# Performance work log

Hardware: AMD Instinct MI355X
Metric: run time of the kernel (lower is better)

Reference implementation:

```python
import jax, jax.numpy as jnp
import numpy as np

B, N, D = 64, 8192, 128
IN, OUT, H = 64, 64, 512
NH_R, NH_W = 4, 4
GD_R = D + 6          # k, beta, g, s(3), gamma
GD_W = 3 * D + 6      # + erase, add
LSTM_IN = IN + OUT + NH_R * D
EPS = 1e-10


def setup_inputs() -> dict:
    key = jax.random.key(0)
    ks = jax.random.split(key, 18)
    f32 = jnp.float32

    def nrm(k, shape, scale=1.0):
        return (jax.random.normal(k, shape) * scale).astype(f32)

    mem_dev = 1.0 / float(np.sqrt(N + D))   # matches NTMMemory.initialize_memory scale
    return {
        'x_input': nrm(ks[0], (B, IN)),
        'prev_y': nrm(ks[1], (B, OUT)),
        'prev_read': nrm(ks[2], (B, NH_R * D), 0.1),
        'memory': nrm(ks[3], (B, N, D), mem_dev),
        'prev_w_read': jax.nn.softmax(nrm(ks[4], (B, NH_R, N)), axis=-1),
        'prev_w_write': jax.nn.softmax(nrm(ks[5], (B, NH_W, N)), axis=-1),
        'h0': nrm(ks[6], (B, H), 0.1),
        'c0': nrm(ks[7], (B, H), 0.1),
        'W_ih': nrm(ks[8], (4 * H, LSTM_IN), 1.0 / np.sqrt(LSTM_IN)),
        'W_hh': nrm(ks[9], (4 * H, H), 1.0 / np.sqrt(H)),
        'b_ih': jnp.zeros((4 * H,), f32),
        'b_hh': jnp.zeros((4 * H,), f32),
        'W_rhead': nrm(ks[10], (NH_R * GD_R, H), 1.0 / np.sqrt(H)),
        'b_rhead': jnp.zeros((NH_R * GD_R,), f32),
        'W_whead': nrm(ks[11], (NH_W * GD_W, H), 1.0 / np.sqrt(H)),
        'b_whead': jnp.zeros((NH_W * GD_W,), f32),
        'W_out': nrm(ks[12], (OUT, H + NH_R * D), 1.0 / np.sqrt(H + NH_R * D)),
        'b_out': jnp.zeros((OUT,), f32),
    }


def _address(ctrl, W, b, nh, gd, memory, prev_w):
    """Content + location addressing for nh heads. ctrl:[B,H] -> w:[B,nh,N]."""
    o = (ctrl @ W.T + b).reshape(ctrl.shape[0], nh, gd)
    k = o[..., :D]                                          # [B,nh,D]
    beta = jax.nn.softplus(o[..., D:D + 1])
    g = jax.nn.sigmoid(o[..., D + 1:D + 2])
    s = jax.nn.softmax(jax.nn.softplus(o[..., D + 2:D + 5]), axis=-1)  # 3-way shift
    gamma = 1.0 + jax.nn.softplus(o[..., D + 5:D + 6])
    # batched cosine similarity (replaces triple python loop in source)
    kn = k / (jnp.linalg.norm(k, axis=-1, keepdims=True) + EPS)
    mn = memory / (jnp.linalg.norm(memory, axis=-1, keepdims=True) + EPS)
    sim = jnp.einsum('bhd,bnd->bhn', kn, mn)                # [B,nh,N]
    wc = jax.nn.softmax(beta * sim, axis=-1)
    # interpolation + circular convolution shift (shifts -1,0,+1)
    wg = g * wc + (1.0 - g) * prev_w
    ws = (s[..., 0:1] * jnp.roll(wg, 1, axis=-1)
          + s[..., 1:2] * wg
          + s[..., 2:3] * jnp.roll(wg, -1, axis=-1))
    # sharpening
    wp = ws ** gamma
    w = wp / (jnp.sum(wp, axis=-1, keepdims=True) + EPS)
    return w, o


def reference(x_input, prev_y, prev_read, memory, prev_w_read, prev_w_write,
              h0, c0, W_ih, W_hh, b_ih, b_hh,
              W_rhead, b_rhead, W_whead, b_whead, W_out, b_out):
    # --- controller: one LSTM step (PyTorch gate order i,f,g,o) ---
    ctrl_in = jnp.concatenate([x_input, prev_y, prev_read], axis=-1)   # [B,LSTM_IN]
    gates = ctrl_in @ W_ih.T + b_ih + h0 @ W_hh.T + b_hh               # [B,4H]
    i, f, gg, o = jnp.split(gates, 4, axis=-1)
    c = jax.nn.sigmoid(f) * c0 + jax.nn.sigmoid(i) * jnp.tanh(gg)
    h = jax.nn.sigmoid(o) * jnp.tanh(c)
    # --- write heads: address then erase/add (batched outer products) ---
    w_w, ow = _address(h, W_whead, b_whead, NH_W, GD_W, memory, prev_w_write)
    erase = ow[..., D + 6:2 * D + 6]       # raw slices, as in source _generate_addressing
    add = ow[..., 2 * D + 6:3 * D + 6]
    mem = memory
    for hidx in range(NH_W):               # small fixed head count
        wv = w_w[:, hidx, :, None]         # [B,N,1]
        mem = mem * (1.0 - wv * erase[:, hidx, None, :]) + wv * add[:, hidx, None, :]
    # --- read heads ---
    w_r, _ = _address(h, W_rhead, b_rhead, NH_R, GD_R, mem, prev_w_read)
    r = jnp.einsum('bhn,bnd->bhd', w_r, mem)                # [B,NH_R,D]
    # --- external output fn ---
    ext_in = jnp.concatenate([h, r.reshape(r.shape[0], NH_R * D)], axis=-1)
    y = jnp.tanh(ext_in @ W_out.T + b_out)                  # [B,OUT]
    return (y, mem, h, c, w_r, w_w)
```

## Files before the change

### kernel.cpp

```cpp
#include <hip/hip_runtime.h>
#include <math.h>

#define B 64
#define N 8192
#define D 128
#define H 512
#define NHEAD 4
#define GDW 390
#define GDR 134
#define KL 1152
#define EPSF 1e-10f

__device__ __forceinline__ float softplusf(float x) {
    return x > 20.f ? x : log1pf(expf(x));
}
__device__ __forceinline__ float sigmoidf(float x) {
    return 1.f / (1.f + expf(-x));
}

__global__ void prep_xt(const float* __restrict__ x, const float* __restrict__ py,
                        const float* __restrict__ pr, const float* __restrict__ h0,
                        float* __restrict__ XT) {
    int idx = blockIdx.x * 256 + threadIdx.x;
    if (idx >= KL * B) return;
    int k = idx >> 6, b = idx & 63;
    float v;
    if (k < 64)       v = x[b * 64 + k];
    else if (k < 128) v = py[b * 64 + (k - 64)];
    else if (k < 640) v = pr[b * 512 + (k - 128)];
    else              v = h0[b * 512 + (k - 640)];
    XT[idx] = v;
}

__global__ __launch_bounds__(256) void controller(const float* __restrict__ XT,
        const float* __restrict__ W_ih, const float* __restrict__ W_hh,
        const float* __restrict__ b_ih, const float* __restrict__ b_hh,
        float* __restrict__ gatesT) {
    __shared__ float xs[64 * 64];
    int tid = threadIdx.x;
    int lane = tid & 63;
    int wave = tid >> 6;
    int j0 = blockIdx.x * 16 + wave * 4;
    float acc[4] = {0.f, 0.f, 0.f, 0.f};
    for (int k0 = 0; k0 < KL; k0 += 64) {
        __syncthreads();
        #pragma unroll
        for (int i = 0; i < 16; i++) xs[tid + i * 256] = XT[k0 * 64 + tid + i * 256];
        __syncthreads();
        const float* wp[4];
        #pragma unroll
        for (int jj = 0; jj < 4; jj++) {
            int j = j0 + jj;
            wp[jj] = (k0 < 640) ? (W_ih + j * 640 + k0) : (W_hh + j * 512 + (k0 - 640));
        }
        #pragma unroll 4
        for (int k = 0; k < 64; k++) {
            float xv = xs[k * 64 + lane];
            #pragma unroll
            for (int jj = 0; jj < 4; jj++) acc[jj] = fmaf(wp[jj][k], xv, acc[jj]);
        }
    }
    #pragma unroll
    for (int jj = 0; jj < 4; jj++) {
        int j = j0 + jj;
        gatesT[j * 64 + lane] = acc[jj] + b_ih[j] + b_hh[j];
    }
}

__global__ void lstm_cell(const float* __restrict__ gatesT, const float* __restrict__ c0,
                          float* __restrict__ h_out, float* __restrict__ c_out,
                          float* __restrict__ HT) {
    int tid = blockIdx.x * 256 + threadIdx.x;
    int b = tid >> 9, u = tid & 511;
    float gi = gatesT[u * 64 + b];
    float gf = gatesT[(512 + u) * 64 + b];
    float gg = gatesT[(1024 + u) * 64 + b];
    float go = gatesT[(1536 + u) * 64 + b];
    float c = sigmoidf(gf) * c0[b * 512 + u] + sigmoidf(gi) * tanhf(gg);
    float h = sigmoidf(go) * tanhf(c);
    c_out[b * 512 + u] = c;
    h_out[b * 512 + u] = h;
    HT[u * 64 + b] = h;
}

__global__ __launch_bounds__(256) void head_proj(const float* __restrict__ HT,
        const float* __restrict__ W_w, const float* __restrict__ W_r,
        const float* __restrict__ b_w, const float* __restrict__ b_r,
        float* __restrict__ o_w, float* __restrict__ o_r) {
    __shared__ float xs[64 * 64];
    int tid = threadIdx.x;
    int lane = tid & 63;
    int wave = tid >> 6;
    int j0 = blockIdx.x * 16 + wave * 4;
    float acc[4] = {0.f, 0.f, 0.f, 0.f};
    const float* wp[4];
    #pragma unroll
    for (int jj = 0; jj < 4; jj++) {
        int j = j0 + jj;
        wp[jj] = (j < 1560) ? (W_w + j * 512) : (W_r + (j - 1560) * 512);
    }
    for (int k0 = 0; k0 < 512; k0 += 64) {
        __syncthreads();
        #pragma unroll
        for (int i = 0; i < 16; i++) xs[tid + i * 256] = HT[k0 * 64 + tid + i * 256];
        __syncthreads();
        #pragma unroll 4
        for (int k = 0; k < 64; k++) {
            float xv = xs[k * 64 + lane];
            #pragma unroll
            for (int jj = 0; jj < 4; jj++) acc[jj] = fmaf(wp[jj][k0 + k], xv, acc[jj]);
        }
    }
    #pragma unroll
    for (int jj = 0; jj < 4; jj++) {
        int j = j0 + jj;
        if (j < 1560) o_w[lane * 1560 + j] = acc[jj] + b_w[j];
        else          o_r[lane * 536 + (j - 1560)] = acc[jj] + b_r[j - 1560];
    }
}

__global__ __launch_bounds__(128) void head_params(const float* __restrict__ o_w,
        const float* __restrict__ o_r, float* __restrict__ knw, float* __restrict__ knr,
        float* __restrict__ pw, float* __restrict__ prd, float* __restrict__ rzero) {
    __shared__ float red[2];
    int id = blockIdx.x;
    if (id < 256) rzero[id * 128 + threadIdx.x] = 0.f;
    bool isw = id < 256;
    int bh = isw ? id : id - 256;
    const float* o = isw ? (o_w + (bh >> 2) * 1560 + (bh & 3) * GDW)
                         : (o_r + (bh >> 2) * 536 + (bh & 3) * GDR);
    float* kn = (isw ? knw : knr) + bh * 128;
    float* pp = (isw ? pw : prd) + bh * 6;
    int t = threadIdx.x;
    float kv = o[t];
    float ss = kv * kv;
    #pragma unroll
    for (int m = 1; m < 64; m <<= 1) ss += __shfl_xor(ss, m);
    if ((t & 63) == 0) red[t >> 6] = ss;
    __syncthreads();
    float norm = sqrtf(red[0] + red[1]);
    kn[t] = kv / (norm + EPSF);
    if (t == 0) {
        float beta = softplusf(o[128]);
        float g = sigmoidf(o[129]);
        float s0 = softplusf(o[130]), s1 = softplusf(o[131]), s2 = softplusf(o[132]);
        float mx = fmaxf(s0, fmaxf(s1, s2));
        float e0 = expf(s0 - mx), e1 = expf(s1 - mx), e2 = expf(s2 - mx);
        float inv = 1.f / (e0 + e1 + e2);
        float gamma = 1.f + softplusf(o[133]);
        pp[0] = beta; pp[1] = g; pp[2] = e0 * inv; pp[3] = e1 * inv; pp[4] = e2 * inv; pp[5] = gamma;
    }
}

__global__ __launch_bounds__(256) void sim_write(const float* __restrict__ mem,
        const float* __restrict__ knw, float* __restrict__ sim) {
    int t = threadIdx.x;
    int lane = t & 63;
    int wv = t >> 6;
    int j = lane & 15;
    int u = lane >> 4;
    int b = blockIdx.x >> 7;
    int nb = (blockIdx.x & 127) * 64 + wv * 16 + u;
    float4 k[4][2];
    #pragma unroll
    for (int h = 0; h < 4; h++) {
        #pragma unroll
        for (int s = 0; s < 2; s++)
            k[h][s] = *(const float4*)(knw + (b * 4 + h) * 128 + s * 64 + j * 4);
    }
    #pragma unroll
    for (int it = 0; it < 4; it++) {
        int n = nb + it * 4;
        size_t base = ((size_t)b * N + n) * D + j * 4;
        const float4 m0 = *(const float4*)(mem + base);
        const float4 m1 = *(const float4*)(mem + base + 64);
        float s0 = m0.x*k[0][0].x + m0.y*k[0][0].y + m0.z*k[0][0].z + m0.w*k[0][0].w
                 + m1.x*k[0][1].x + m1.y*k[0][1].y + m1.z*k[0][1].z + m1.w*k[0][1].w;
        float s1 = m0.x*k[1][0].x + m0.y*k[1][0].y + m0.z*k[1][0].z + m0.w*k[1][0].w
                 + m1.x*k[1][1].x + m1.y*k[1][1].y + m1.z*k[1][1].z + m1.w*k[1][1].w;
        float s2 = m0.x*k[2][0].x + m0.y*k[2][0].y + m0.z*k[2][0].z + m0.w*k[2][0].w
                 + m1.x*k[2][1].x + m1.y*k[2][1].y + m1.z*k[2][1].z + m1.w*k[2][1].w;
        float s3 = m0.x*k[3][0].x + m0.y*k[3][0].y + m0.z*k[3][0].z + m0.w*k[3][0].w
                 + m1.x*k[3][1].x + m1.y*k[3][1].y + m1.z*k[3][1].z + m1.w*k[3][1].w;
        float nn = m0.x*m0.x + m0.y*m0.y + m0.z*m0.z + m0.w*m0.w
                 + m1.x*m1.x + m1.y*m1.y + m1.z*m1.z + m1.w*m1.w;
        s0 += __shfl_xor(s0, 1); s1 += __shfl_xor(s1, 1);
        s2 += __shfl_xor(s2, 1); s3 += __shfl_xor(s3, 1); nn += __shfl_xor(nn, 1);
        float p01 = (j & 1) ? s1 : s0;
        float p23 = (j & 1) ? s3 : s2;
        p01 += __shfl_xor(p01, 2); p23 += __shfl_xor(p23, 2); nn += __shfl_xor(nn, 2);
        float q = (j & 2) ? p23 : p01;
        q += __shfl_xor(q, 4);  nn += __shfl_xor(nn, 4);
        q += __shfl_xor(q, 8);  nn += __shfl_xor(nn, 8);
        if (j < 4) sim[((size_t)(b * 4 + j)) * N + n] = q / (sqrtf(nn) + EPSF);
    }
}

__global__ __launch_bounds__(512) void addr_finalize(const float* __restrict__ sim,
        const float* __restrict__ prev_w, const float* __restrict__ par,
        float* __restrict__ w_out) {
    __shared__ float buf[N];
    __shared__ float pbuf[N];
    __shared__ float red[8];
    int bh = blockIdx.x;
    int t = threadIdx.x;
    const float* s = sim + (size_t)bh * N;
    const float* pw = prev_w + (size_t)bh * N;
    float beta = par[bh * 6 + 0], g = par[bh * 6 + 1];
    float s0 = par[bh * 6 + 2], s1 = par[bh * 6 + 3], s2 = par[bh * 6 + 4];
    float gamma = par[bh * 6 + 5];
    float mx = -INFINITY;
    for (int i = t; i < N; i += 512) {
        float e = beta * s[i];
        buf[i] = e;
        mx = fmaxf(mx, e);
    }
    #pragma unroll
    for (int m = 1; m < 64; m <<= 1) mx = fmaxf(mx, __shfl_xor(mx, m));
    if ((t & 63) == 0) red[t >> 6] = mx;
    __syncthreads();
    mx = red[0];
    #pragma unroll
    for (int kk = 1; kk < 8; kk++) mx = fmaxf(mx, red[kk]);
    float sum = 0.f;
    for (int i = t; i < N; i += 512) {
        float v = expf(buf[i] - mx);
        buf[i] = v;
        sum += v;
    }
    #pragma unroll
    for (int m = 1; m < 64; m <<= 1) sum += __shfl_xor(sum, m);
    __syncthreads();
    if ((t & 63) == 0) red[t >> 6] = sum;
    __syncthreads();
    sum = red[0] + red[1] + red[2] + red[3] + red[4] + red[5] + red[6] + red[7];
    float inv = 1.f / sum;
    for (int i = t; i < N; i += 512) buf[i] = g * (buf[i] * inv) + (1.f - g) * pw[i];
    __syncthreads();
    float psum = 0.f;
    for (int i = t; i < N; i += 512) {
        float wsv = s0 * buf[(i + N - 1) & (N - 1)] + s1 * buf[i] + s2 * buf[(i + 1) & (N - 1)];
        float pv = powf(wsv, gamma);
        pbuf[i] = pv;
        psum += pv;
    }
    #pragma unroll
    for (int m = 1; m < 64; m <<= 1) psum += __shfl_xor(psum, m);
    __syncthreads();
    if ((t & 63) == 0) red[t >> 6] = psum;
    __syncthreads();
    psum = red[0] + red[1] + red[2] + red[3] + red[4] + red[5] + red[6] + red[7];
    float rinv = 1.f / (psum + EPSF);
    for (int i = t; i < N; i += 512) w_out[(size_t)bh * N + i] = pbuf[i] * rinv;
}

__global__ __launch_bounds__(256) void mem_update(const float* __restrict__ mem_in,
        const float* __restrict__ o_w, const float* __restrict__ w_w,
        const float* __restrict__ knr, float* __restrict__ mem_out,
        float* __restrict__ simr) {
    __shared__ float wlds[4][64];
    int t = threadIdx.x;
    int l = t & 31;
    int rg = t >> 5;
    int b = blockIdx.x >> 7;
    int n0 = (blockIdx.x & 127) * 64;
    {
        int h = t >> 6, idx = t & 63;
        wlds[h][idx] = w_w[((size_t)(b * 4 + h)) * N + n0 + idx];
    }
    float4 e[4], a[4], kr[4];
    #pragma unroll
    for (int h = 0; h < 4; h++) {
        const float* ob = o_w + b * 1560 + h * GDW;
        e[h].x = ob[134 + l * 4 + 0]; e[h].y = ob[134 + l * 4 + 1];
        e[h].z = ob[134 + l * 4 + 2]; e[h].w = ob[134 + l * 4 + 3];
        a[h].x = ob[262 + l * 4 + 0]; a[h].y = ob[262 + l * 4 + 1];
        a[h].z = ob[262 + l * 4 + 2]; a[h].w = ob[262 + l * 4 + 3];
        kr[h] = *(const float4*)(knr + (b * 4 + h) * 128 + l * 4);
    }
    __syncthreads();
    for (int it = 0; it < 8; it++) {
        int n = n0 + it * 8 + rg;
        size_t base = ((size_t)b * N + n) * D + l * 4;
        float4 m = *(const float4*)(mem_in + base);
        #pragma unroll
        for (int h = 0; h < 4; h++) {
            float wv = wlds[h][it * 8 + rg];
            m.x = m.x * (1.f - wv * e[h].x) + wv * a[h].x;
            m.y = m.y * (1.f - wv * e[h].y) + wv * a[h].y;
            m.z = m.z * (1.f - wv * e[h].z) + wv * a[h].z;
            m.w = m.w * (1.f - wv * e[h].w) + wv * a[h].w;
        }
        *(float4*)(mem_out + base) = m;
        float s0 = m.x * kr[0].x + m.y * kr[0].y + m.z * kr[0].z + m.w * kr[0].w;
        float s1 = m.x * kr[1].x + m.y * kr[1].y + m.z * kr[1].z + m.w * kr[1].w;
        float s2 = m.x * kr[2].x + m.y * kr[2].y + m.z * kr[2].z + m.w * kr[2].w;
        float s3 = m.x * kr[3].x + m.y * kr[3].y + m.z * kr[3].z + m.w * kr[3].w;
        float nn = m.x * m.x + m.y * m.y + m.z * m.z + m.w * m.w;
        s0 += __shfl_xor(s0, 1); s1 += __shfl_xor(s1, 1);
        s2 += __shfl_xor(s2, 1); s3 += __shfl_xor(s3, 1); nn += __shfl_xor(nn, 1);
        float p01 = (l & 1) ? s1 : s0;
        float p23 = (l & 1) ? s3 : s2;
        p01 += __shfl_xor(p01, 2); p23 += __shfl_xor(p23, 2); nn += __shfl_xor(nn, 2);
        float q = (l & 2) ? p23 : p01;
        q += __shfl_xor(q, 4); nn += __shfl_xor(nn, 4);
        float z = (l & 4) ? nn : q;
        z += __shfl_xor(z, 8);
        z += __shfl_xor(z, 16);
        float nnv = __shfl_xor(z, 4);
        if (l < 4) simr[((size_t)(b * 4 + l)) * N + n] = z / (sqrtf(nnv) + EPSF);
    }
}

__global__ __launch_bounds__(256) void read_vec(const float* __restrict__ mem,
        const float* __restrict__ w_r, float* __restrict__ r) {
    __shared__ float lds[8 * 512];
    __shared__ float wlds[4][512];
    int t = threadIdx.x;
    int l = t & 31;
    int rg = t >> 5;
    int b = blockIdx.x >> 4;
    int n0 = (blockIdx.x & 15) * 512;
    for (int i = t; i < 2048; i += 256) {
        int h = i >> 9, idx = i & 511;
        wlds[h][idx] = w_r[((size_t)(b * 4 + h)) * N + n0 + idx];
    }
    __syncthreads();
    float4 acc[4];
    #pragma unroll
    for (int h = 0; h < 4; h++) acc[h] = make_float4(0.f, 0.f, 0.f, 0.f);
    for (int it = 0; it < 64; it++) {
        int nl = it * 8 + rg;
        const float4 m = *(const float4*)(mem + ((size_t)b * N + n0 + nl) * D + l * 4);
        #pragma unroll
        for (int h = 0; h < 4; h++) {
            float wv = wlds[h][nl];
            acc[h].x += wv * m.x;
            acc[h].y += wv * m.y;
            acc[h].z += wv * m.z;
            acc[h].w += wv * m.w;
        }
    }
    #pragma unroll
    for (int h = 0; h < 4; h++) *(float4*)(lds + rg * 512 + h * 128 + l * 4) = acc[h];
    __syncthreads();
    for (int o = t; o < 512; o += 256) {
        float sum = 0.f;
        #pragma unroll
        for (int g2 = 0; g2 < 8; g2++) sum += lds[g2 * 512 + o];
        atomicAdd(&r[b * 512 + o], sum);
    }
}

__global__ __launch_bounds__(64) void out_y(const float* __restrict__ h,
        const float* __restrict__ r, const float* __restrict__ W_out,
        const float* __restrict__ b_out, float* __restrict__ y) {
    int b = blockIdx.x >> 6;
    int j = blockIdx.x & 63;
    int l = threadIdx.x;
    float acc = 0.f;
    #pragma unroll
    for (int kk = 0; kk < 16; kk++) {
        int k = l + kk * 64;
        float x = (k < 512) ? h[b * 512 + k] : r[b * 512 + (k - 512)];
        acc = fmaf(W_out[j * 1024 + k], x, acc);
    }
    #pragma unroll
    for (int m = 1; m < 64; m <<= 1) acc += __shfl_xor(acc, m);
    if (l == 0) y[b * 64 + j] = tanhf(acc + b_out[j]);
}

extern "C" void kernel_launch(void* const* d_in, const int* in_sizes, int n_in,
                              void* d_out, int out_size, void* d_ws, size_t ws_size,
                              hipStream_t stream) {
    const float* x_input      = (const float*)d_in[0];
    const float* prev_y       = (const float*)d_in[1];
    const float* prev_read    = (const float*)d_in[2];
    const float* memory       = (const float*)d_in[3];
    const float* prev_w_read  = (const float*)d_in[4];
    const float* prev_w_write = (const float*)d_in[5];
    const float* h0           = (const float*)d_in[6];
    const float* c0           = (const float*)d_in[7];
    const float* W_ih         = (const float*)d_in[8];
    const float* W_hh         = (const float*)d_in[9];
    const float* b_ih         = (const float*)d_in[10];
    const float* b_hh         = (const float*)d_in[11];
    const float* W_rhead      = (const float*)d_in[12];
    const float* b_rhead      = (const float*)d_in[13];
    const float* W_whead      = (const float*)d_in[14];
    const float* b_whead      = (const float*)d_in[15];
    const float* W_out        = (const float*)d_in[16];
    const float* b_out        = (const float*)d_in[17];

    float* out = (float*)d_out;
    float* y_o   = out;
    float* mem_o = out + 4096;
    float* h_o   = out + 4096 + 67108864;
    float* c_o   = h_o + 32768;
    float* wr_o  = c_o + 32768;
    float* ww_o  = wr_o + 2097152;

    float* ws     = (float*)d_ws;
    float* XT     = ws;
    float* HT     = XT + 73728;
    float* gatesT = HT + 32768;
    float* o_w    = gatesT + 131072;
    float* o_r    = o_w + 99840;
    float* knw    = o_r + 34304;
    float* knr    = knw + 32768;
    float* pw     = knr + 32768;
    float* prd    = pw + 1536;
    float* sim_w  = prd + 1536;
    float* sim_r  = sim_w + 2097152;
    float* r_ws   = sim_r + 2097152;

    prep_xt<<<288, 256, 0, stream>>>(x_input, prev_y, prev_read, h0, XT);
    controller<<<128, 256, 0, stream>>>(XT, W_ih, W_hh, b_ih, b_hh, gatesT);
    lstm_cell<<<128, 256, 0, stream>>>(gatesT, c0, h_o, c_o, HT);
    head_proj<<<131, 256, 0, stream>>>(HT, W_whead, W_rhead, b_whead, b_rhead, o_w, o_r);
    head_params<<<512, 128, 0, stream>>>(o_w, o_r, knw, knr, pw, prd, r_ws);
    sim_write<<<8192, 256, 0, stream>>>(memory, knw, sim_w);
    addr_finalize<<<256, 512, 0, stream>>>(sim_w, prev_w_write, pw, ww_o);
    mem_update<<<8192, 256, 0, stream>>>(memory, o_w, ww_o, knr, mem_o, sim_r);
    addr_finalize<<<256, 512, 0, stream>>>(sim_r, prev_w_read, prd, wr_o);
    read_vec<<<1024, 256, 0, stream>>>(mem_o, wr_o, r_ws);
    out_y<<<4096, 64, 0, stream>>>(h_o, r_ws, W_out, b_out, y_o);
}
```

Measured before the change: 756.5 us.

## Fuse memory addressing, update and read stages into one cooperative persistent kernel

Replaces the five-kernel sequence (write similarity, write addressing, memory update, read addressing, read vector) with one cooperative kernel of 1024 blocks, separated by grid syncs. Each block owns a fixed 512-row slice of one batch's memory, so a block reads back the same slice in later phases, which may hit in cache, and four launches are removed. The addressing routine also drops to 256 threads and recomputes powf in its last pass instead of keeping a second 32 KB LDS buffer, which cuts shared-memory use. The costs are grid-wide barriers, only 256 of 1024 blocks doing work in the addressing phases, and a reliance on cooperative launch, with an occupancy check and a fallback to the old kernels.

```diff
diff --git a/kernel.cpp b/kernel.cpp
--- a/kernel.cpp
+++ b/kernel.cpp
@@ -1,5 +1,8 @@
 #include <hip/hip_runtime.h>
+#include <hip/hip_cooperative_groups.h>
 #include <math.h>
+
+namespace cg = cooperative_groups;
 
 #define B 64
 #define N 8192
@@ -149,6 +152,208 @@
         float inv = 1.f / (e0 + e1 + e2);
         float gamma = 1.f + softplusf(o[133]);
         pp[0] = beta; pp[1] = g; pp[2] = e0 * inv; pp[3] = e1 * inv; pp[4] = e2 * inv; pp[5] = gamma;
+    }
+}
+
+__device__ void addr_phase(float* __restrict__ buf, float* __restrict__ red,
+                           const float* __restrict__ sim, const float* __restrict__ prevw,
+                           const float* __restrict__ par, float* __restrict__ w_out,
+                           int bh, int t) {
+    const float* s = sim + (size_t)bh * N;
+    const float* pwp = prevw + (size_t)bh * N;
+    float beta = par[bh * 6 + 0], g = par[bh * 6 + 1];
+    float s0 = par[bh * 6 + 2], s1 = par[bh * 6 + 3], s2 = par[bh * 6 + 4];
+    float gamma = par[bh * 6 + 5];
+    float mx = -INFINITY;
+    for (int i = t; i < N; i += 256) {
+        float e = beta * s[i];
+        buf[i] = e;
+        mx = fmaxf(mx, e);
+    }
+    #pragma unroll
+    for (int m = 1; m < 64; m <<= 1) mx = fmaxf(mx, __shfl_xor(mx, m));
+    if ((t & 63) == 0) red[t >> 6] = mx;
+    __syncthreads();
+    mx = fmaxf(fmaxf(red[0], red[1]), fmaxf(red[2], red[3]));
+    float sum = 0.f;
+    for (int i = t; i < N; i += 256) {
+        float v = expf(buf[i] - mx);
+        buf[i] = v;
+        sum += v;
+    }
+    #pragma unroll
+    for (int m = 1; m < 64; m <<= 1) sum += __shfl_xor(sum, m);
+    __syncthreads();
+    if ((t & 63) == 0) red[t >> 6] = sum;
+    __syncthreads();
+    sum = red[0] + red[1] + red[2] + red[3];
+    float inv = 1.f / sum;
+    for (int i = t; i < N; i += 256) buf[i] = g * (buf[i] * inv) + (1.f - g) * pwp[i];
+    __syncthreads();
+    float psum = 0.f;
+    for (int i = t; i < N; i += 256) {
+        float wsv = s0 * buf[(i + N - 1) & (N - 1)] + s1 * buf[i] + s2 * buf[(i + 1) & (N - 1)];
+        psum += powf(wsv, gamma);
+    }
+    #pragma unroll
+    for (int m = 1; m < 64; m <<= 1) psum += __shfl_xor(psum, m);
+    __syncthreads();
+    if ((t & 63) == 0) red[t >> 6] = psum;
+    __syncthreads();
+    psum = red[0] + red[1] + red[2] + red[3];
+    float rinv = 1.f / (psum + EPSF);
+    for (int i = t; i < N; i += 256) {
+        float wsv = s0 * buf[(i + N - 1) & (N - 1)] + s1 * buf[i] + s2 * buf[(i + 1) & (N - 1)];
+        w_out[(size_t)bh * N + i] = powf(wsv, gamma) * rinv;
+    }
+}
+
+__global__ __launch_bounds__(256, 4) void ntm_coop(
+        const float* __restrict__ mem_in, const float* __restrict__ knw,
+        const float* __restrict__ knr, const float* __restrict__ o_w,
+        const float* __restrict__ pw, const float* __restrict__ prd,
+        const float* __restrict__ pww, const float* __restrict__ pwr,
+        float* __restrict__ sim_w, float* __restrict__ sim_r,
+        float* __restrict__ ww_o, float* __restrict__ wr_o,
+        float* __restrict__ mem_o, float* __restrict__ r_ws) {
+    cg::grid_group grid = cg::this_grid();
+    __shared__ float smem[8448];
+    int t = threadIdx.x;
+    int blk = blockIdx.x;
+    int b = blk >> 4, part = blk & 15;
+    int n0 = part * 512;
+
+    {
+        int lane = t & 63, wv2 = t >> 6, j = lane & 15, u = lane >> 4;
+        float4 k[4][2];
+        #pragma unroll
+        for (int h = 0; h < 4; h++) {
+            #pragma unroll
+            for (int sgm = 0; sgm < 2; sgm++)
+                k[h][sgm] = *(const float4*)(knw + (b * 4 + h) * 128 + sgm * 64 + j * 4);
+        }
+        int rbase = n0 + wv2 * 16 + u;
+        for (int q = 0; q < 32; q++) {
+            int n = rbase + (q >> 2) * 64 + (q & 3) * 4;
+            size_t base = ((size_t)b * N + n) * D + j * 4;
+            const float4 m0 = *(const float4*)(mem_in + base);
+            const float4 m1 = *(const float4*)(mem_in + base + 64);
+            float s0 = m0.x*k[0][0].x + m0.y*k[0][0].y + m0.z*k[0][0].z + m0.w*k[0][0].w
+                     + m1.x*k[0][1].x + m1.y*k[0][1].y + m1.z*k[0][1].z + m1.w*k[0][1].w;
+            float s1 = m0.x*k[1][0].x + m0.y*k[1][0].y + m0.z*k[1][0].z + m0.w*k[1][0].w
+                     + m1.x*k[1][1].x + m1.y*k[1][1].y + m1.z*k[1][1].z + m1.w*k[1][1].w;
+            float s2 = m0.x*k[2][0].x + m0.y*k[2][0].y + m0.z*k[2][0].z + m0.w*k[2][0].w
+                     + m1.x*k[2][1].x + m1.y*k[2][1].y + m1.z*k[2][1].z + m1.w*k[2][1].w;
+            float s3 = m0.x*k[3][0].x + m0.y*k[3][0].y + m0.z*k[3][0].z + m0.w*k[3][0].w
+                     + m1.x*k[3][1].x + m1.y*k[3][1].y + m1.z*k[3][1].z + m1.w*k[3][1].w;
+            float nn = m0.x*m0.x + m0.y*m0.y + m0.z*m0.z + m0.w*m0.w
+                     + m1.x*m1.x + m1.y*m1.y + m1.z*m1.z + m1.w*m1.w;
+            s0 += __shfl_xor(s0, 1); s1 += __shfl_xor(s1, 1);
+            s2 += __shfl_xor(s2, 1); s3 += __shfl_xor(s3, 1); nn += __shfl_xor(nn, 1);
+            float p01 = (j & 1) ? s1 : s0;
+            float p23 = (j & 1) ? s3 : s2;
+            p01 += __shfl_xor(p01, 2); p23 += __shfl_xor(p23, 2); nn += __shfl_xor(nn, 2);
+            float qv = (j & 2) ? p23 : p01;
+            qv += __shfl_xor(qv, 4);  nn += __shfl_xor(nn, 4);
+            qv += __shfl_xor(qv, 8);  nn += __shfl_xor(nn, 8);
+            if (j < 4) sim_w[((size_t)(b * 4 + j)) * N + n] = qv / (sqrtf(nn) + EPSF);
+        }
+    }
+    __threadfence();
+    grid.sync();
+
+    if (blk < 256) addr_phase(smem, smem + 8192, sim_w, pww, pw, ww_o, blk, t);
+    __threadfence();
+    grid.sync();
+
+    {
+        for (int i = t; i < 2048; i += 256) {
+            int h = i >> 9, idx = i & 511;
+            smem[i] = ww_o[((size_t)(b * 4 + h)) * N + n0 + idx];
+        }
+        int l = t & 31, rg = t >> 5;
+        float4 e[4], a[4], kr[4];
+        #pragma unroll
+        for (int h = 0; h < 4; h++) {
+            const float* ob = o_w + b * 1560 + h * GDW;
+            e[h].x = ob[134 + l * 4 + 0]; e[h].y = ob[134 + l * 4 + 1];
+            e[h].z = ob[134 + l * 4 + 2]; e[h].w = ob[134 + l * 4 + 3];
+            a[h].x = ob[262 + l * 4 + 0]; a[h].y = ob[262 + l * 4 + 1];
+            a[h].z = ob[262 + l * 4 + 2]; a[h].w = ob[262 + l * 4 + 3];
+            kr[h] = *(const float4*)(knr + (b * 4 + h) * 128 + l * 4);
+        }
+        __syncthreads();
+        for (int it = 0; it < 64; it++) {
+            int nl = it * 8 + rg;
+            int n = n0 + nl;
+            size_t base = ((size_t)b * N + n) * D + l * 4;
+            float4 m = *(const float4*)(mem_in + base);
+            #pragma unroll
+            for (int h = 0; h < 4; h++) {
+                float wv = smem[h * 512 + nl];
+                m.x = m.x * (1.f - wv * e[h].x) + wv * a[h].x;
+                m.y = m.y * (1.f - wv * e[h].y) + wv * a[h].y;
+                m.z = m.z * (1.f - wv * e[h].z) + wv * a[h].z;
+                m.w = m.w * (1.f - wv * e[h].w) + wv * a[h].w;
+            }
+            *(float4*)(mem_o + base) = m;
+            float s0 = m.x * kr[0].x + m.y * kr[0].y + m.z * kr[0].z + m.w * kr[0].w;
+            float s1 = m.x * kr[1].x + m.y * kr[1].y + m.z * kr[1].z + m.w * kr[1].w;
+            float s2 = m.x * kr[2].x + m.y * kr[2].y + m.z * kr[2].z + m.w * kr[2].w;
+            float s3 = m.x * kr[3].x + m.y * kr[3].y + m.z * kr[3].z + m.w * kr[3].w;
+            float nn = m.x * m.x + m.y * m.y + m.z * m.z + m.w * m.w;
+            s0 += __shfl_xor(s0, 1); s1 += __shfl_xor(s1, 1);
+            s2 += __shfl_xor(s2, 1); s3 += __shfl_xor(s3, 1); nn += __shfl_xor(nn, 1);
+            float p01 = (l & 1) ? s1 : s0;
+            float p23 = (l & 1) ? s3 : s2;
+            p01 += __shfl_xor(p01, 2); p23 += __shfl_xor(p23, 2); nn += __shfl_xor(nn, 2);
+            float qv = (l & 2) ? p23 : p01;
+            qv += __shfl_xor(qv, 4); nn += __shfl_xor(nn, 4);
+            float z = (l & 4) ? nn : qv;
+            z += __shfl_xor(z, 8);
+            z += __shfl_xor(z, 16);
+            float nnv = __shfl_xor(z, 4);
+            if (l < 4) sim_r[((size_t)(b * 4 + l)) * N + n] = z / (sqrtf(nnv) + EPSF);
+        }
+    }
+    __threadfence();
+    grid.sync();
+
+    if (blk < 256) addr_phase(smem, smem + 8192, sim_r, pwr, prd, wr_o, blk, t);
+    __threadfence();
+    grid.sync();
+
+    {
+        for (int i = t; i < 2048; i += 256) {
+            int h = i >> 9, idx = i & 511;
+            smem[4096 + i] = wr_o[((size_t)(b * 4 + h)) * N + n0 + idx];
+        }
+        __syncthreads();
+        int l = t & 31, rg = t >> 5;
+        float4 acc[4];
+        #pragma unroll
+        for (int h = 0; h < 4; h++) acc[h] = make_float4(0.f, 0.f, 0.f, 0.f);
+        for (int it = 0; it < 64; it++) {
+            int nl = it * 8 + rg;
+            const float4 m = *(const float4*)(mem_o + ((size_t)b * N + n0 + nl) * D + l * 4);
+            #pragma unroll
+            for (int h = 0; h < 4; h++) {
+                float wv = smem[4096 + h * 512 + nl];
+                acc[h].x += wv * m.x;
+                acc[h].y += wv * m.y;
+                acc[h].z += wv * m.z;
+                acc[h].w += wv * m.w;
+            }
+        }
+        #pragma unroll
+        for (int h = 0; h < 4; h++) *(float4*)(smem + rg * 512 + h * 128 + l * 4) = acc[h];
+        __syncthreads();
+        for (int o = t; o < 512; o += 256) {
+            float sum = 0.f;
+            #pragma unroll
+            for (int g2 = 0; g2 < 8; g2++) sum += smem[g2 * 512 + o];
+            atomicAdd(&r_ws[b * 512 + o], sum);
+        }
     }
 }
 
@@ -196,62 +401,12 @@
     }
 }
 
-__global__ __launch_bounds__(512) void addr_finalize(const float* __restrict__ sim,
+__global__ __launch_bounds__(256) void addr_finalize(const float* __restrict__ sim,
         const float* __restrict__ prev_w, const float* __restrict__ par,
         float* __restrict__ w_out) {
     __shared__ float buf[N];
-    __shared__ float pbuf[N];
-    __shared__ float red[8];
-    int bh = blockIdx.x;
-    int t = threadIdx.x;
-    const float* s = sim + (size_t)bh * N;
-    const float* pw = prev_w + (size_t)bh * N;
-    float beta = par[bh * 6 + 0], g = par[bh * 6 + 1];
-    float s0 = par[bh * 6 + 2], s1 = par[bh * 6 + 3], s2 = par[bh * 6 + 4];
-    float gamma = par[bh * 6 + 5];
-    float mx = -INFINITY;
-    for (int i = t; i < N; i += 512) {
-        float e = beta * s[i];
-        buf[i] = e;
-        mx = fmaxf(mx, e);
-    }
-    #pragma unroll
-    for (int m = 1; m < 64; m <<= 1) mx = fmaxf(mx, __shfl_xor(mx, m));
-    if ((t & 63) == 0) red[t >> 6] = mx;
-    __syncthreads();
-    mx = red[0];
-    #pragma unroll
-    for (int kk = 1; kk < 8; kk++) mx = fmaxf(mx, red[kk]);
-    float sum = 0.f;
-    for (int i = t; i < N; i += 512) {
-        float v = expf(buf[i] - mx);
-        buf[i] = v;
-        sum += v;
-    }
-    #pragma unroll
-    for (int m = 1; m < 64; m <<= 1) sum += __shfl_xor(sum, m);
-    __syncthreads();
-    if ((t & 63) == 0) red[t >> 6] = sum;
-    __syncthreads();
-    sum = red[0] + red[1] + red[2] + red[3] + red[4] + red[5] + red[6] + red[7];
-    float inv = 1.f / sum;
-    for (int i = t; i < N; i += 512) buf[i] = g * (buf[i] * inv) + (1.f - g) * pw[i];
-    __syncthreads();
-    float psum = 0.f;
-    for (int i = t; i < N; i += 512) {
-        float wsv = s0 * buf[(i + N - 1) & (N - 1)] + s1 * buf[i] + s2 * buf[(i + 1) & (N - 1)];
-        float pv = powf(wsv, gamma);
-        pbuf[i] = pv;
-        psum += pv;
-    }
-    #pragma unroll
-    for (int m = 1; m < 64; m <<= 1) psum += __shfl_xor(psum, m);
-    __syncthreads();
-    if ((t & 63) == 0) red[t >> 6] = psum;
-    __syncthreads();
-    psum = red[0] + red[1] + red[2] + red[3] + red[4] + red[5] + red[6] + red[7];
-    float rinv = 1.f / (psum + EPSF);
-    for (int i = t; i < N; i += 512) w_out[(size_t)bh * N + i] = pbuf[i] * rinv;
+    __shared__ float red[4];
+    addr_phase(buf, red, sim, prev_w, par, w_out, blockIdx.x, threadIdx.x);
 }
 
 __global__ __launch_bounds__(256) void mem_update(const float* __restrict__ mem_in,
@@ -419,10 +574,31 @@
     lstm_cell<<<128, 256, 0, stream>>>(gatesT, c0, h_o, c_o, HT);
     head_proj<<<131, 256, 0, stream>>>(HT, W_whead, W_rhead, b_whead, b_rhead, o_w, o_r);
     head_params<<<512, 128, 0, stream>>>(o_w, o_r, knw, knr, pw, prd, r_ws);
-    sim_write<<<8192, 256, 0, stream>>>(memory, knw, sim_w);
-    addr_finalize<<<256, 512, 0, stream>>>(sim_w, prev_w_write, pw, ww_o);
-    mem_update<<<8192, 256, 0, stream>>>(memory, o_w, ww_o, knr, mem_o, sim_r);
-    addr_finalize<<<256, 512, 0, stream>>>(sim_r, prev_w_read, prd, wr_o);
-    read_vec<<<1024, 256, 0, stream>>>(mem_o, wr_o, r_ws);
+
+    static int coop_state = -1;
+    if (coop_state < 0) {
+        int nb = 0;
+        hipError_t e = hipOccupancyMaxActiveBlocksPerMultiprocessor(&nb, ntm_coop, 256, 0);
+        coop_state = (e == hipSuccess && nb >= 4) ? 1 : 0;
+    }
+    bool used_coop = false;
+    if (coop_state == 1) {
+        void* args[14] = {
+            (void*)&memory, (void*)&knw, (void*)&knr, (void*)&o_w,
+            (void*)&pw, (void*)&prd, (void*)&prev_w_write, (void*)&prev_w_read,
+            (void*)&sim_w, (void*)&sim_r, (void*)&ww_o, (void*)&wr_o,
+            (void*)&mem_o, (void*)&r_ws };
+        hipError_t e = hipLaunchCooperativeKernel(ntm_coop, dim3(1024), dim3(256),
+                                                  args, 0, stream);
+        if (e == hipSuccess) used_coop = true;
+        else coop_state = 0;
+    }
+    if (!used_coop) {
+        sim_write<<<8192, 256, 0, stream>>>(memory, knw, sim_w);
+        addr_finalize<<<256, 256, 0, stream>>>(sim_w, prev_w_write, pw, ww_o);
+        mem_update<<<8192, 256, 0, stream>>>(memory, o_w, ww_o, knr, mem_o, sim_r);
+        addr_finalize<<<256, 256, 0, stream>>>(sim_r, prev_w_read, prd, wr_o);
+        read_vec<<<1024, 256, 0, stream>>>(mem_o, wr_o, r_ws);
+    }
     out_y<<<4096, 64, 0, stream>>>(h_o, r_ws, W_out, b_out, y_o);
 }
```

New measurement: 799.1 us. 5.6% more time.
